# Performance work log

Hardware: AMD Instinct MI355X
Metric: run time of the kernel (lower is better)

Reference implementation:

```python
import jax, jax.numpy as jnp
import numpy as np

B, K, D, C = 16384, 8, 128, 128


def setup_inputs() -> dict:
    key = jax.random.key(0)
    k1, k2, k3, k4, k5 = jax.random.split(key, 5)
    return {
        "graph_embeddings": jax.random.normal(k1, (B, D), dtype=jnp.float32),
        "retrieval_embeddings": jax.random.normal(k2, (B, K, D), dtype=jnp.float32),
        "W_adapter": jax.random.normal(k3, (D, D), dtype=jnp.float32) / np.sqrt(D),
        "W_pred": jax.random.normal(k4, (D, C), dtype=jnp.float32) / np.sqrt(D),
        "b_pred": jnp.zeros((C,), dtype=jnp.float32),
        "labels": jax.random.randint(k5, (B, K), 0, C, dtype=jnp.int64).astype(jnp.int32),
    }


def reference(graph_embeddings, retrieval_embeddings, W_adapter, W_pred, b_pred, labels):
    # g_label = Softmax(dim=1)(graph_pred_linear(graph_embeddings))   [B, C]
    g_label = jax.nn.softmax(graph_embeddings @ W_pred + b_pred, axis=1)

    # concat_H = cat([graph_embeddings] + retrievals, -1).view(B, K+1, D)
    concat_H = jnp.concatenate([graph_embeddings[:, None, :], retrieval_embeddings], axis=1)  # [B, K+1, D]

    # adapter: bilinear attention scores, softmax over the K+1 candidates
    scores = jnp.einsum("bd,de,bme->bm", graph_embeddings, W_adapter, concat_H)  # [B, K+1]
    attention = jax.nn.softmax(scores, axis=1)

    # generic-dataset branch of the per-sample loop, vectorized:
    #   adjusted[b] = attn[b,0] * g_label[b]
    #   adjusted[b, labels[b,k]] += attn[b, k]   for k in range(K)
    # (note: faithful to the original, which indexes attention[b][k], not k+1)
    one_hot = jax.nn.one_hot(labels, C, dtype=g_label.dtype)  # [B, K, C]
    adjusted_label = attention[:, :1] * g_label + jnp.einsum("bk,bkc->bc", attention[:, :K], one_hot)
    return adjusted_label
```

## Files before the change

kernel.cpp:

```cpp
#include <hip/hip_runtime.h>


#define SB      8
#define THREADS 256

__global__ __launch_bounds__(THREADS)
void graph_retrieval_fused(const float* __restrict__ G,
                           const float* __restrict__ R,
                           const float* __restrict__ Wa,
                           const float* __restrict__ Wp,
                           const float* __restrict__ bp,
                           const int*   __restrict__ labels,
                           float* __restrict__ out)
{
    __shared__ float g_lds[SB * 128];
    __shared__ float t_lds[SB * 128];
    __shared__ float logit_lds[SB * 132];
    __shared__ float attn_lds[SB * 8];
    __shared__ float stat_m[SB], stat_iz[SB];
    __shared__ int   lab_lds[SB * 8];

    const int tid = threadIdx.x;
    const int b0  = blockIdx.x * SB;

    ((float4*)g_lds)[tid] = ((const float4*)(G + (size_t)b0 * 128))[tid];
    if (tid < SB * 8) lab_lds[tid] = labels[b0 * 8 + tid];
    __syncthreads();

    const int c     = tid & 127;
    const int h     = tid >> 7;
    const int sbase = h * 4;

    float t_acc[4], l_acc[4];
    {
        const float bias = bp[c];
        #pragma unroll
        for (int i = 0; i < 4; ++i) { t_acc[i] = 0.f; l_acc[i] = bias; }

        for (int d0 = 0; d0 < 128; d0 += 8) {
            float wa[8], wp8[8];
            #pragma unroll
            for (int j = 0; j < 8; ++j) {
                wa[j]  = Wa[(d0 + j) * 128 + c];
                wp8[j] = Wp[(d0 + j) * 128 + c];
            }
            #pragma unroll
            for (int i = 0; i < 4; ++i) {
                const float4 ga = *(const float4*)&g_lds[(sbase + i) * 128 + d0];
                const float4 gb = *(const float4*)&g_lds[(sbase + i) * 128 + d0 + 4];
                t_acc[i] += ga.x * wa[0] + ga.y * wa[1] + ga.z * wa[2] + ga.w * wa[3]
                          + gb.x * wa[4] + gb.y * wa[5] + gb.z * wa[6] + gb.w * wa[7];
                l_acc[i] += ga.x * wp8[0] + ga.y * wp8[1] + ga.z * wp8[2] + ga.w * wp8[3]
                          + gb.x * wp8[4] + gb.y * wp8[5] + gb.z * wp8[6] + gb.w * wp8[7];
            }
        }
        #pragma unroll
        for (int i = 0; i < 4; ++i) {
            t_lds[(sbase + i) * 128 + c]     = t_acc[i];
            logit_lds[(sbase + i) * 132 + c] = l_acc[i];
        }
    }
    __syncthreads();

    {
        const int wv   = tid >> 6;
        const int lane = tid & 63;
        const int s0   = wv * 2;

        const float2 e0 = *(const float2*)&logit_lds[s0 * 132 + 2 * lane];
        const float2 e1 = *(const float2*)&logit_lds[(s0 + 1) * 132 + 2 * lane];
        float m0 = fmaxf(e0.x, e0.y), m1 = fmaxf(e1.x, e1.y);
        #pragma unroll
        for (int off = 32; off > 0; off >>= 1) {
            m0 = fmaxf(m0, __shfl_xor(m0, off, 64));
            m1 = fmaxf(m1, __shfl_xor(m1, off, 64));
        }
        float z0 = __expf(e0.x - m0) + __expf(e0.y - m0);
        float z1 = __expf(e1.x - m1) + __expf(e1.y - m1);
        #pragma unroll
        for (int off = 32; off > 0; off >>= 1) {
            z0 += __shfl_xor(z0, off, 64);
            z1 += __shfl_xor(z1, off, 64);
        }
        if (lane == 0) {
            stat_m[s0]      = m0;  stat_iz[s0]      = 1.f / z0;
            stat_m[s0 + 1]  = m1;  stat_iz[s0 + 1]  = 1.f / z1;
        }

        float scA[9], scB[9];
        {
            const float2 tA = *(const float2*)&t_lds[s0 * 128 + 2 * lane];
            const float2 tB = *(const float2*)&t_lds[(s0 + 1) * 128 + 2 * lane];
            const float2 gA = *(const float2*)&g_lds[s0 * 128 + 2 * lane];
            const float2 gB = *(const float2*)&g_lds[(s0 + 1) * 128 + 2 * lane];
            scA[0] = tA.x * gA.x + tA.y * gA.y;
            scB[0] = tB.x * gB.x + tB.y * gB.y;
            const float2* RrA = (const float2*)(R + (size_t)(b0 + s0) * 8 * 128);
            const float2* RrB = (const float2*)(R + (size_t)(b0 + s0 + 1) * 8 * 128);
            #pragma unroll
            for (int m = 1; m < 9; ++m) {
                const float2 ra = RrA[(m - 1) * 64 + lane];
                const float2 rb = RrB[(m - 1) * 64 + lane];
                scA[m] = tA.x * ra.x + tA.y * ra.y;
                scB[m] = tB.x * rb.x + tB.y * rb.y;
            }
        }
        #pragma unroll
        for (int off = 32; off > 0; off >>= 1) {
            #pragma unroll
            for (int m = 0; m < 9; ++m) {
                scA[m] += __shfl_xor(scA[m], off, 64);
                scB[m] += __shfl_xor(scB[m], off, 64);
            }
        }
        float mxA = scA[0], mxB = scB[0];
        #pragma unroll
        for (int m = 1; m < 9; ++m) { mxA = fmaxf(mxA, scA[m]); mxB = fmaxf(mxB, scB[m]); }
        float eA[9], eB[9], sA = 0.f, sB = 0.f;
        #pragma unroll
        for (int m = 0; m < 9; ++m) {
            eA[m] = __expf(scA[m] - mxA); sA += eA[m];
            eB[m] = __expf(scB[m] - mxB); sB += eB[m];
        }
        const float iA = 1.f / sA, iB = 1.f / sB;
        if (lane == 0) {
            #pragma unroll
            for (int m = 0; m < 8; ++m) {
                attn_lds[s0 * 8 + m]       = eA[m] * iA;
                attn_lds[(s0 + 1) * 8 + m] = eB[m] * iB;
            }
        }
    }
    __syncthreads();

    #pragma unroll
    for (int i = 0; i < 4; ++i) {
        const int s = sbase + i;
        const float gl = __expf(l_acc[i] - stat_m[s]) * stat_iz[s];
        float val = attn_lds[s * 8 + 0] * gl;
        #pragma unroll
        for (int k = 0; k < 8; ++k)
            val += (lab_lds[s * 8 + k] == c) ? attn_lds[s * 8 + k] : 0.f;
        out[(size_t)(b0 + s) * 128 + c] = val;
    }
}

extern "C" void kernel_launch(void* const* d_in, const int* in_sizes, int n_in,
                              void* d_out, int out_size, void* d_ws, size_t ws_size,
                              hipStream_t stream) {
    const float* G      = (const float*)d_in[0];
    const float* R      = (const float*)d_in[1];
    const float* Wa     = (const float*)d_in[2];
    const float* Wp     = (const float*)d_in[3];
    const float* bpred  = (const float*)d_in[4];
    const int*   labels = (const int*)d_in[5];
    float*       o      = (float*)d_out;

    const int B = in_sizes[0] / 128;
    dim3 grid(B / SB), block(THREADS);
    hipLaunchKernelGGL(graph_retrieval_fused, grid, block, 0, stream,
                       G, R, Wa, Wp, bpred, labels, o);
}
```

Before: 137.0 us.

## Prefetch retrieval rows at kernel start and double-buffer weight loads

Each wave now loads its retrieval-embedding rows into registers at the very start of the kernel, so the largest global read overlaps the G load and the projection GEMV instead of sitting after a barrier. The weight-column loads in the projection loop are software-pipelined with two register buffers and a fully unrolled loop, and launch bounds now request 4 blocks per CU. This hides memory latency in a bandwidth-bound kernel, but it raises register pressure (32 extra floats held for R plus the duplicated weight buffers), which the occupancy hint may force into spills.

```diff
diff --git a/kernel.cpp b/kernel.cpp
--- a/kernel.cpp
+++ b/kernel.cpp
@@ -4,7 +4,7 @@
 #define SB      8
 #define THREADS 256
 
-__global__ __launch_bounds__(THREADS)
+__global__ __launch_bounds__(THREADS, 4)
 void graph_retrieval_fused(const float* __restrict__ G,
                            const float* __restrict__ R,
                            const float* __restrict__ Wa,
@@ -20,8 +20,22 @@
     __shared__ float stat_m[SB], stat_iz[SB];
     __shared__ int   lab_lds[SB * 8];
 
-    const int tid = threadIdx.x;
-    const int b0  = blockIdx.x * SB;
+    const int tid  = threadIdx.x;
+    const int b0   = blockIdx.x * SB;
+    const int wv   = tid >> 6;
+    const int lane = tid & 63;
+    const int s0   = wv * 2;
+
+    float2 rA[8], rB[8];
+    {
+        const float2* RrA = (const float2*)(R + (size_t)(b0 + s0) * 1024);
+        const float2* RrB = RrA + 512;
+        #pragma unroll
+        for (int m = 0; m < 8; ++m) {
+            rA[m] = RrA[m * 64 + lane];
+            rB[m] = RrB[m * 64 + lane];
+        }
+    }
 
     ((float4*)g_lds)[tid] = ((const float4*)(G + (size_t)b0 * 128))[tid];
     if (tid < SB * 8) lab_lds[tid] = labels[b0 * 8 + tid];
@@ -37,21 +51,43 @@
         #pragma unroll
         for (int i = 0; i < 4; ++i) { t_acc[i] = 0.f; l_acc[i] = bias; }
 
-        for (int d0 = 0; d0 < 128; d0 += 8) {
-            float wa[8], wp8[8];
+        float waA[8], wpA[8], waB[8], wpB[8];
+        #pragma unroll
+        for (int j = 0; j < 8; ++j) {
+            waA[j] = Wa[j * 128 + c];
+            wpA[j] = Wp[j * 128 + c];
+        }
+
+        #pragma unroll
+        for (int d0 = 0; d0 < 128; d0 += 16) {
             #pragma unroll
             for (int j = 0; j < 8; ++j) {
-                wa[j]  = Wa[(d0 + j) * 128 + c];
-                wp8[j] = Wp[(d0 + j) * 128 + c];
+                waB[j] = Wa[(d0 + 8 + j) * 128 + c];
+                wpB[j] = Wp[(d0 + 8 + j) * 128 + c];
             }
             #pragma unroll
             for (int i = 0; i < 4; ++i) {
                 const float4 ga = *(const float4*)&g_lds[(sbase + i) * 128 + d0];
                 const float4 gb = *(const float4*)&g_lds[(sbase + i) * 128 + d0 + 4];
-                t_acc[i] += ga.x * wa[0] + ga.y * wa[1] + ga.z * wa[2] + ga.w * wa[3]
-                          + gb.x * wa[4] + gb.y * wa[5] + gb.z * wa[6] + gb.w * wa[7];
-                l_acc[i] += ga.x * wp8[0] + ga.y * wp8[1] + ga.z * wp8[2] + ga.w * wp8[3]
-                          + gb.x * wp8[4] + gb.y * wp8[5] + gb.z * wp8[6] + gb.w * wp8[7];
+                t_acc[i] += ga.x * waA[0] + ga.y * waA[1] + ga.z * waA[2] + ga.w * waA[3]
+                          + gb.x * waA[4] + gb.y * waA[5] + gb.z * waA[6] + gb.w * waA[7];
+                l_acc[i] += ga.x * wpA[0] + ga.y * wpA[1] + ga.z * wpA[2] + ga.w * wpA[3]
+                          + gb.x * wpA[4] + gb.y * wpA[5] + gb.z * wpA[6] + gb.w * wpA[7];
+            }
+            const int nxt = (d0 + 16) & 127;
+            #pragma unroll
+            for (int j = 0; j < 8; ++j) {
+                waA[j] = Wa[(nxt + j) * 128 + c];
+                wpA[j] = Wp[(nxt + j) * 128 + c];
+            }
+            #pragma unroll
+            for (int i = 0; i < 4; ++i) {
+                const float4 ga = *(const float4*)&g_lds[(sbase + i) * 128 + d0 + 8];
+                const float4 gb = *(const float4*)&g_lds[(sbase + i) * 128 + d0 + 12];
+                t_acc[i] += ga.x * waB[0] + ga.y * waB[1] + ga.z * waB[2] + ga.w * waB[3]
+                          + gb.x * waB[4] + gb.y * waB[5] + gb.z * waB[6] + gb.w * waB[7];
+                l_acc[i] += ga.x * wpB[0] + ga.y * wpB[1] + ga.z * wpB[2] + ga.w * wpB[3]
+                          + gb.x * wpB[4] + gb.y * wpB[5] + gb.z * wpB[6] + gb.w * wpB[7];
             }
         }
         #pragma unroll
@@ -63,10 +99,6 @@
     __syncthreads();
 
     {
-        const int wv   = tid >> 6;
-        const int lane = tid & 63;
-        const int s0   = wv * 2;
-
         const float2 e0 = *(const float2*)&logit_lds[s0 * 132 + 2 * lane];
         const float2 e1 = *(const float2*)&logit_lds[(s0 + 1) * 132 + 2 * lane];
         float m0 = fmaxf(e0.x, e0.y), m1 = fmaxf(e1.x, e1.y);
@@ -83,8 +115,8 @@
             z1 += __shfl_xor(z1, off, 64);
         }
         if (lane == 0) {
-            stat_m[s0]      = m0;  stat_iz[s0]      = 1.f / z0;
-            stat_m[s0 + 1]  = m1;  stat_iz[s0 + 1]  = 1.f / z1;
+            stat_m[s0]     = m0;  stat_iz[s0]     = 1.f / z0;
+            stat_m[s0 + 1] = m1;  stat_iz[s0 + 1] = 1.f / z1;
         }
 
         float scA[9], scB[9];
@@ -95,14 +127,10 @@
             const float2 gB = *(const float2*)&g_lds[(s0 + 1) * 128 + 2 * lane];
             scA[0] = tA.x * gA.x + tA.y * gA.y;
             scB[0] = tB.x * gB.x + tB.y * gB.y;
-            const float2* RrA = (const float2*)(R + (size_t)(b0 + s0) * 8 * 128);
-            const float2* RrB = (const float2*)(R + (size_t)(b0 + s0 + 1) * 8 * 128);
             #pragma unroll
             for (int m = 1; m < 9; ++m) {
-                const float2 ra = RrA[(m - 1) * 64 + lane];
-                const float2 rb = RrB[(m - 1) * 64 + lane];
-                scA[m] = tA.x * ra.x + tA.y * ra.y;
-                scB[m] = tB.x * rb.x + tB.y * rb.y;
+                scA[m] = tA.x * rA[m - 1].x + tA.y * rA[m - 1].y;
+                scB[m] = tB.x * rB[m - 1].x + tB.y * rB[m - 1].y;
             }
         }
         #pragma unroll
```

Result: no change. 136.0 us (-0.8%).
